# Performance work log

Measured on AMD Instinct MI355X. Metric: run time of the kernel, lower is better.

## Reference

```python
import jax, jax.numpy as jnp
from jax import lax
import numpy as np

DN = ('NCDHW', 'OIDHW', 'NCDHW')
EPS = 1e-3  # BatchNorm1d eps=0.001
GRID = (41, 512, 512)  # spatial_shape [40,512,512] + [1,0,0]


def _block(x, mask, w, gamma, beta, rmean, rvar, stride, padding):
    # Regular (non-submanifold) sparse conv computes the same values as a dense
    # conv on the zero-filled grid; active OUTPUT sites are exactly those reached
    # by any active input site through the kernel window. BN+ReLU act only on
    # active sites (inactive sites stay exactly 0), hence the mask multiply.
    y = lax.conv_general_dilated(x, w, stride, padding, dimension_numbers=DN)
    k1 = jnp.ones((1, 1) + w.shape[2:], x.dtype)
    m = lax.conv_general_dilated(mask, k1, stride, padding, dimension_numbers=DN)
    m = (m > 0).astype(x.dtype)
    inv = gamma / jnp.sqrt(rvar + EPS)
    scale = inv.reshape(1, -1, 1, 1, 1)
    shift = (beta - rmean * inv).reshape(1, -1, 1, 1, 1)
    return jax.nn.relu(y * scale + shift) * m, m


def setup_inputs() -> dict:
    key = jax.random.key(0)
    NV, B = 120000, 2
    kf, kb, kz, ky, kx, kp = jax.random.split(key, 6)
    voxel_features = jax.random.normal(kf, (NV, 3), jnp.float32)
    coors = jnp.stack([
        jax.random.randint(kb, (NV,), 0, B, jnp.int32),
        jax.random.randint(kz, (NV,), 0, 40, jnp.int32),
        jax.random.randint(ky, (NV,), 0, 512, jnp.int32),
        jax.random.randint(kx, (NV,), 0, 512, jnp.int32)], axis=1)
    inp = {"voxel_features": voxel_features, "coors": coors, "batch_size": B}
    chans = [(3, 16, (3, 3, 3)), (16, 32, (3, 3, 3)), (32, 64, (3, 3, 3)), (64, 64, (3, 1, 1))]
    for i, (ci, co, k) in enumerate(chans, 1):
        kw, kg, kbb, km, kv = jax.random.split(jax.random.fold_in(kp, i), 5)
        fan = ci * k[0] * k[1] * k[2]
        inp[f"w{i}"] = jax.random.normal(kw, (co, ci) + k, jnp.float32) / np.sqrt(fan).astype(np.float32)
        inp[f"g{i}"] = jax.random.uniform(kg, (co,), jnp.float32, 0.5, 1.5)
        inp[f"bb{i}"] = jax.random.normal(kbb, (co,), jnp.float32) * 0.1
        inp[f"rm{i}"] = jax.random.normal(km, (co,), jnp.float32) * 0.1
        inp[f"rv{i}"] = jax.random.uniform(kv, (co,), jnp.float32, 0.5, 1.5)
    return inp


def reference(voxel_features, coors, batch_size,
              w1, g1, bb1, rm1, rv1,
              w2, g2, bb2, rm2, rv2,
              w3, g3, bb3, rm3, rv3,
              w4, g4, bb4, rm4, rv4):
    D, H, W = GRID
    C = voxel_features.shape[1]
    b, z, y, x = coors[:, 0], coors[:, 1], coors[:, 2], coors[:, 3]
    dense = jnp.zeros((batch_size, C, D, H, W), voxel_features.dtype)
    dense = dense.at[b, :, z, y, x].add(voxel_features)  # scatter voxels to grid
    mask = jnp.zeros((batch_size, 1, D, H, W), voxel_features.dtype).at[b, 0, z, y, x].set(1.0)
    h, m = _block(dense, mask, w1, g1, bb1, rm1, rv1, (2, 2, 2), [(1, 1), (1, 1), (1, 1)])
    h, m = _block(h, m, w2, g2, bb2, rm2, rv2, (2, 2, 2), [(1, 1), (1, 1), (1, 1)])
    h, m = _block(h, m, w3, g3, bb3, rm3, rv3, (2, 2, 2), [(0, 0), (1, 1), (1, 1)])
    h, m = _block(h, m, w4, g4, bb4, rm4, rv4, (2, 1, 1), [(0, 0), (0, 0), (0, 0)])
    N, Co, Dd, Hh, Ww = h.shape  # [B, 64, 2, 64, 64]
    return h.reshape(N, Co * Dd, Hh, Ww)
```

## Files before the change

kernel.cpp:

```cpp
#include <hip/hip_runtime.h>

#define EPS 1e-3f


static __device__ __forceinline__ unsigned f2bf(float f) {
    unsigned u = __float_as_uint(f);
    return (u + 0x7FFFu + ((u >> 16) & 1u)) >> 16;
}

typedef _Float16 f16x8 __attribute__((ext_vector_type(8)));
typedef float f32x4 __attribute__((ext_vector_type(4)));
typedef float f32x16 __attribute__((ext_vector_type(16)));

__global__ __launch_bounds__(256) void repack_prezero(
    const float* __restrict__ g1, const float* __restrict__ b1,
    const float* __restrict__ rm1, const float* __restrict__ rv1,
    const float* __restrict__ w2, const float* __restrict__ g2, const float* __restrict__ b2,
    const float* __restrict__ rm2, const float* __restrict__ rv2,
    const float* __restrict__ w3, const float* __restrict__ g3, const float* __restrict__ b3,
    const float* __restrict__ rm3, const float* __restrict__ rv3,
    const float* __restrict__ w4, const float* __restrict__ g4, const float* __restrict__ b4,
    const float* __restrict__ rm4, const float* __restrict__ rv4,
    _Float16* __restrict__ wB2, _Float16* __restrict__ wB3,
    _Float16* __restrict__ wB4, float* __restrict__ shb,
    const int* __restrict__ coors, int NV, unsigned short* __restrict__ y1)
{
    if (blockIdx.x >= 321) {
        const int i = (blockIdx.x - 321) * 256 + threadIdx.x;
        if (i < NV) {
            const int b = coors[4 * i + 0];
            const int z = coors[4 * i + 1];
            const int y = coors[4 * i + 2];
            const int x = coors[4 * i + 3];
            int ozv[2], nz = 0, oyv[2], ny = 0, oxv[2], nx = 0;
#pragma unroll
            for (int k = 0; k < 3; ++k) {
                int t = z + 1 - k;
                if (t >= 0 && !(t & 1)) { int o = t >> 1; if (o < 21) ozv[nz++] = o; }
            }
#pragma unroll
            for (int k = 0; k < 3; ++k) {
                int t = y + 1 - k;
                if (t >= 0 && !(t & 1)) { int o = t >> 1; if (o < 256) oyv[ny++] = o; }
            }
#pragma unroll
            for (int k = 0; k < 3; ++k) {
                int t = x + 1 - k;
                if (t >= 0 && !(t & 1)) { int o = t >> 1; if (o < 256) oxv[nx++] = o; }
            }
            const uint4 zz = {0u, 0u, 0u, 0u};
            for (int a = 0; a < nz; ++a)
                for (int bb = 0; bb < ny; ++bb)
                    for (int c = 0; c < nx; ++c) {
                        const int sp = ozv[a] * 65536 + oyv[bb] * 256 + oxv[c];
                        uint4* p = (uint4*)(y1 + (size_t)(b * 1376256 + sp) * 16);
                        p[0] = zz;
                        p[1] = zz;
                    }
        }
        asm volatile("s_waitcnt vmcnt(0)" ::: "memory");
        return;
    }

    const int i = blockIdx.x * 256 + threadIdx.x;
    if (i < 13824) {
        const int j = i & 7, lane = (i >> 3) & 63, tap = i >> 9;
        const int oc = lane & 31;
        const int cin = (lane >> 5) * 8 + j;
        const float inv = g2[oc] * rsqrtf(rv2[oc] + EPS);
        wB2[i] = (_Float16)(w2[(oc * 16 + cin) * 27 + tap] * inv);
    } else if (i >= 14336 && i < 69632) {
        const int j2 = i - 14336;
        const int j = j2 & 7, lane = (j2 >> 3) & 63, t = (j2 >> 9) & 3, tap = j2 >> 11;
        const int q = lane >> 4, n = lane & 15;
        const int oc = t * 16 + n;
        const int cin = q * 8 + j;
        const float inv = g3[oc] * rsqrtf(rv3[oc] + EPS);
        wB3[j2] = (_Float16)(w3[(oc * 32 + cin) * 27 + tap] * inv);
    } else if (i >= 69632 && i < 81920) {
        const int j2 = i - 69632;
        const int j = j2 & 7, lane = (j2 >> 3) & 63, t = (j2 >> 9) & 3, c = j2 >> 11;
        const int q = lane >> 4, n = lane & 15;
        const int oc = t * 16 + n;
        const int k = c * 32 + q * 8 + j;
        const int dz = k >> 6, cin = k & 63;
        const float inv = g4[oc] * rsqrtf(rv4[oc] + EPS);
        wB4[j2] = (_Float16)(w4[(oc * 64 + cin) * 3 + dz] * inv);
    } else if (i >= 81920 && i < 82112) {
        const int j = i - 81920;
        if (j < 32) {
            const float inv = g2[j] * rsqrtf(rv2[j] + EPS);
            shb[j] = b2[j] - rm2[j] * inv;
        } else if (j < 96) {
            const int o = j - 32;
            const float inv = g3[o] * rsqrtf(rv3[o] + EPS);
            shb[j] = b3[o] - rm3[o] * inv;
        } else if (j < 160) {
            const int o = j - 96;
            const float inv = g4[o] * rsqrtf(rv4[o] + EPS);
            shb[j] = b4[o] - rm4[o] * inv;
        } else if (j < 176) {
            const int o = j - 160;
            shb[j] = g1[o] * rsqrtf(rv1[o] + EPS);
        } else if (j < 192) {
            const int o = j - 176;
            const float inv = g1[o] * rsqrtf(rv1[o] + EPS);
            shb[j] = b1[o] - rm1[o] * inv;
        }
    }
}

__global__ __launch_bounds__(256) void scatter_l1(
    const float* __restrict__ vf, const int* __restrict__ coors, int NV,
    const float* __restrict__ w1, const float* __restrict__ shb,
    unsigned short* __restrict__ y1, unsigned char* __restrict__ m1)
{
    __shared__ float ws[16 * 3 * 27];
    for (int e = threadIdx.x; e < 16 * 3 * 27; e += 256)
        ws[e] = w1[e] * shb[160 + e / 81];
    __syncthreads();

    const int gid = blockIdx.x * 256 + threadIdx.x;
    const int i = gid >> 3;
    const int oc2 = gid & 7;
    if (i < NV) {
        const int oc = oc2 * 2;

        const int b = coors[4 * i + 0];
        const int z = coors[4 * i + 1];
        const int y = coors[4 * i + 2];
        const int x = coors[4 * i + 3];
        const float f0 = vf[3 * i + 0];
        const float f1 = vf[3 * i + 1];
        const float f2 = vf[3 * i + 2];

        int ozv[2], kzv[2], nz = 0;
        int oyv[2], kyv[2], ny = 0;
        int oxv[2], kxv[2], nx = 0;
#pragma unroll
        for (int k = 0; k < 3; ++k) {
            int t = z + 1 - k;
            if (t >= 0 && !(t & 1)) { int o = t >> 1; if (o < 21) { ozv[nz] = o; kzv[nz] = k; ++nz; } }
        }
#pragma unroll
        for (int k = 0; k < 3; ++k) {
            int t = y + 1 - k;
            if (t >= 0 && !(t & 1)) { int o = t >> 1; if (o < 256) { oyv[ny] = o; kyv[ny] = k; ++ny; } }
        }
#pragma unroll
        for (int k = 0; k < 3; ++k) {
            int t = x + 1 - k;
            if (t >= 0 && !(t & 1)) { int o = t >> 1; if (o < 256) { oxv[nx] = o; kxv[nx] = k; ++nx; } }
        }

        for (int a = 0; a < nz; ++a)
            for (int bb = 0; bb < ny; ++bb)
                for (int c = 0; c < nx; ++c) {
                    const int oz = ozv[a], oy = oyv[bb], ox = oxv[c];
                    const int tap = (kzv[a] * 3 + kyv[bb]) * 3 + kxv[c];
                    const int sp = oz * 65536 + oy * 256 + ox;
                    if (oc2 == 0) m1[b * 1376256 + sp] = 1;
                    const float s0 = ws[oc * 81 + tap] * f0 + ws[oc * 81 + 27 + tap] * f1 +
                                     ws[oc * 81 + 54 + tap] * f2;
                    const float s1 = ws[(oc + 1) * 81 + tap] * f0 +
                                     ws[(oc + 1) * 81 + 27 + tap] * f1 +
                                     ws[(oc + 1) * 81 + 54 + tap] * f2;
                    const unsigned pk = f2bf(s0) | (f2bf(s1) << 16);
                    unsigned* addr = (unsigned*)(y1 + (size_t)(b * 1376256 + sp) * 16 +
                                                 oc2 * 2);
                    asm volatile("global_atomic_pk_add_bf16 %0, %1, off"
                                 : : "v"(addr), "v"(pk) : "memory");
                }
    }
    asm volatile("s_waitcnt vmcnt(0)" ::: "memory");
}

__global__ __launch_bounds__(256) void h1_pass(
    uint4* __restrict__ y1b, const unsigned char* __restrict__ m1,
    const float* __restrict__ shb, float* __restrict__ m2)
{
    const int idx = blockIdx.x * 256 + threadIdx.x;
    if (m1[idx]) {
        uint4 u0 = y1b[idx * 2], u1 = y1b[idx * 2 + 1];
        const unsigned d[8] = {u0.x, u0.y, u0.z, u0.w, u1.x, u1.y, u1.z, u1.w};
        unsigned o[8];
#pragma unroll
        for (int j = 0; j < 8; ++j) {
            const int c0 = 2 * j;
            const float vlo = __uint_as_float(d[j] << 16);
            const float vhi = __uint_as_float(d[j] & 0xFFFF0000u);
            const float v0 = fmaxf(vlo + shb[176 + c0], 0.f);
            const float v1 = fmaxf(vhi + shb[176 + c0 + 1], 0.f);
            o[j] = __builtin_bit_cast(unsigned, __builtin_amdgcn_cvt_pkrtz(v0, v1));
        }
        uint4 w0, w1;
        w0.x = o[0]; w0.y = o[1]; w0.z = o[2]; w0.w = o[3];
        w1.x = o[4]; w1.y = o[5]; w1.z = o[6]; w1.w = o[7];
        y1b[idx * 2] = w0;
        y1b[idx * 2 + 1] = w1;
    } else {
        const uint4 zz = {0u, 0u, 0u, 0u};
        y1b[idx * 2] = zz;
        y1b[idx * 2 + 1] = zz;
    }

    if (idx < 360448) {
        const int b = idx / 180224;
        const int r = idx - b * 180224;
        const int oz = r >> 14, r2 = r & 16383, oy = r2 >> 7, ox = r2 & 127;
        const int iz0 = 2 * oz - 1, iyb = 2 * oy - 1, ixb = 2 * ox - 1;
        unsigned msum = 0;
#pragma unroll
        for (int kz = 0; kz < 3; ++kz) {
            const int iz = iz0 + kz;
#pragma unroll
            for (int ky = 0; ky < 3; ++ky) {
                const int iy = iyb + ky;
#pragma unroll
                for (int kx = 0; kx < 3; ++kx) {
                    const int ix = ixb + kx;
                    if ((unsigned)iz < 21u && (unsigned)iy < 256u &&
                        (unsigned)ix < 256u)
                        msum |= m1[b * 1376256 + iz * 65536 + iy * 256 + ix];
                }
            }
        }
        m2[idx] = msum ? 1.f : 0.f;
    }
}

__global__ __launch_bounds__(256) void build_m3(
    const float* __restrict__ m2, float* __restrict__ m3)
{
    const int idx = blockIdx.x * 256 + threadIdx.x;
    if (idx >= 40960) return;
    const int b = idx / 20480;
    const int r = idx - b * 20480;
    const int oz = r >> 12, r2 = r & 4095, oy = r2 >> 6, ox = r2 & 63;
    const int iz0 = 2 * oz, iyb = 2 * oy - 1, ixb = 2 * ox - 1;

    float msum = 0.f;
#pragma unroll
    for (int kz = 0; kz < 3; ++kz) {
        const int iz = iz0 + kz;
#pragma unroll
        for (int ky = 0; ky < 3; ++ky) {
            const int iy = iyb + ky;
#pragma unroll
            for (int kx = 0; kx < 3; ++kx) {
                const int ix = ixb + kx;
                if ((unsigned)iy < 128u && (unsigned)ix < 128u)
                    msum += m2[b * 180224 + iz * 16384 + iy * 128 + ix];
            }
        }
    }
    m3[idx] = msum > 0.f ? 1.f : 0.f;
}

__global__ __launch_bounds__(256) __attribute__((amdgpu_waves_per_eu(4, 8)))
void conv_l2(
    const unsigned char* __restrict__ h1,
    const uint4* __restrict__ wB2,
    const float* __restrict__ m2, const float* __restrict__ shb,
    _Float16* __restrict__ h2h)
{
    const int tid = threadIdx.x;
    const int gw = blockIdx.x * 4 + (tid >> 6);
    const int lane = tid & 63;
    const int m = lane & 31, h = lane >> 5;

    const int plane = gw >> 9;
    const int rem = gw & 511;
    const int oy = rem >> 2;
    const int ox0 = (rem & 3) * 32;
    const int b = plane / 11, oz = plane % 11;
    const int iz0 = 2 * oz - 1, iyb = 2 * oy - 1;
    const int ixm = 2 * (ox0 + m) - 1;
    const int bbase = b * 1376256;
    const int qoff = h * 16;

    f32x16 acc;
#pragma unroll
    for (int r = 0; r < 16; ++r) acc[r] = 0.f;

    uint4 buf[13];
    bool  val[13];
#pragma unroll
    for (int t = 0; t < 13; ++t) {
        const int kz = t / 9, ky = (t / 3) % 3, kx = t % 3;
        const int iz = iz0 + kz, iy = iyb + ky, ix = ixm + kx;
        const bool v = (unsigned)iz < 21u && (unsigned)iy < 256u &&
                       (unsigned)ix < 256u;
        const int cell = bbase + iz * 65536 + iy * 256 + ix;
        buf[t] = *(const uint4*)(h1 + (v ? (cell * 32 + qoff) : 0));
        val[t] = v;
    }

#pragma unroll
    for (int tap = 0; tap < 27; ++tap) {
        const int s = tap % 13;
        uint4 ua = buf[s];
        if (!val[s]) { ua.x = 0; ua.y = 0; ua.z = 0; ua.w = 0; }
        if (tap + 13 < 27) {
            const int t2 = tap + 13;
            const int kz = t2 / 9, ky = (t2 / 3) % 3, kx = t2 % 3;
            const int iz = iz0 + kz, iy = iyb + ky, ix = ixm + kx;
            const bool v = (unsigned)iz < 21u && (unsigned)iy < 256u &&
                           (unsigned)ix < 256u;
            const int cell = bbase + iz * 65536 + iy * 256 + ix;
            buf[s] = *(const uint4*)(h1 + (v ? (cell * 32 + qoff) : 0));
            val[s] = v;
        }
        const f16x8 af = __builtin_bit_cast(f16x8, ua);
        const f16x8 bf = __builtin_bit_cast(f16x8, wB2[tap * 64 + lane]);
        acc = __builtin_amdgcn_mfma_f32_32x32x16_f16(af, bf, acc, 0, 0, 0);
    }

    const int oc = lane & 31;
#pragma unroll
    for (int r = 0; r < 16; ++r) {
        const int row = (r & 3) + 8 * (r >> 2) + 4 * h;
        const int px = ox0 + row;
        const int spo = oz * 16384 + oy * 128 + px;
        const float mv = m2[b * 180224 + spo];
        const size_t cbase = (size_t)(b * 180224 + spo) * 32;
        h2h[cbase + oc] = (_Float16)(fmaxf(acc[r] + shb[oc], 0.f) * mv);
    }
}

__global__ __launch_bounds__(256) __attribute__((amdgpu_waves_per_eu(4, 8)))
void conv_l3(
    const unsigned char* __restrict__ h2h,
    const uint4* __restrict__ wB3,
    const float* __restrict__ m3, const float* __restrict__ shb,
    _Float16* __restrict__ h3h)
{
    const int tid = threadIdx.x;
    const int gw = blockIdx.x * 4 + (tid >> 6);
    const int lane = tid & 63;
    const int m = lane & 15, q = lane >> 4;

    const int plane = gw >> 8;
    const int rem = gw & 255;
    const int oy = rem >> 2;
    const int ox0 = (rem & 3) * 16;
    const int b = plane / 5, oz = plane % 5;
    const int iz0 = 2 * oz, iyb = 2 * oy - 1;
    const int ixm = 2 * (ox0 + m) - 1;
    const int bbase = b * 180224;
    const int qoff = q * 16;

    f32x4 acc[4];
#pragma unroll
    for (int t = 0; t < 4; ++t) acc[t] = (f32x4){0.f, 0.f, 0.f, 0.f};

    uint4 buf[9];
    bool  val[9];
#pragma unroll
    for (int t = 0; t < 9; ++t) {
        const int ky = (t / 3) % 3, kx = t % 3;
        const int iz = iz0 + t / 9, iy = iyb + ky, ix = ixm + kx;
        const bool v = (unsigned)iy < 128u && (unsigned)ix < 128u;
        const int cell = bbase + iz * 16384 + iy * 128 + ix;
        buf[t] = *(const uint4*)(h2h + (v ? (cell * 64 + qoff) : 0));
        val[t] = v;
    }

#pragma unroll
    for (int tap = 0; tap < 27; ++tap) {
        const int s = tap % 9;
        uint4 ua = buf[s];
        if (!val[s]) { ua.x = 0; ua.y = 0; ua.z = 0; ua.w = 0; }
        if (tap + 9 < 27) {
            const int t2 = tap + 9;
            const int kz = t2 / 9, ky = (t2 / 3) % 3, kx = t2 % 3;
            const int iz = iz0 + kz, iy = iyb + ky, ix = ixm + kx;
            const bool v = (unsigned)iy < 128u && (unsigned)ix < 128u;
            const int cell = bbase + iz * 16384 + iy * 128 + ix;
            buf[s] = *(const uint4*)(h2h + (v ? (cell * 64 + qoff) : 0));
            val[s] = v;
        }
        const f16x8 af = __builtin_bit_cast(f16x8, ua);
#pragma unroll
        for (int t = 0; t < 4; ++t) {
            const f16x8 bf = __builtin_bit_cast(f16x8, wB3[(tap * 4 + t) * 64 + lane]);
            acc[t] = __builtin_amdgcn_mfma_f32_16x16x32_f16(af, bf, acc[t], 0, 0, 0);
        }
    }

    const int n = lane & 15;
#pragma unroll
    for (int r = 0; r < 4; ++r) {
        const int px = ox0 + q * 4 + r;
        const int spo = oz * 4096 + oy * 64 + px;
        const float mv = m3[b * 20480 + spo];
        const size_t cb = (size_t)(b * 20480 + spo) * 64;
#pragma unroll
        for (int t = 0; t < 4; ++t) {
            const int oc = t * 16 + n;
            h3h[cb + oc] = (_Float16)(fmaxf(acc[t][r] + shb[32 + oc], 0.f) * mv);
        }
    }
}

__global__ __launch_bounds__(256) __attribute__((amdgpu_waves_per_eu(4, 8)))
void conv_l4(
    const unsigned char* __restrict__ h3h,
    const uint4* __restrict__ wB4,
    const float* __restrict__ m3, const float* __restrict__ shb,
    float* __restrict__ out)
{
    const int tid = threadIdx.x;
    const int gw = blockIdx.x * 4 + (tid >> 6);
    const int lane = tid & 63;
    const int m = lane & 15, q = lane >> 4;

    const int b = gw >> 9, od = (gw >> 8) & 1;
    const int oy = (gw >> 2) & 63, ox0 = (gw & 3) * 16;
    const int cellbase = (b * 5 + 2 * od) * 4096 + oy * 64 + ox0 + m;

    f32x4 acc[4];
#pragma unroll
    for (int t = 0; t < 4; ++t) acc[t] = (f32x4){0.f, 0.f, 0.f, 0.f};

#pragma unroll
    for (int c = 0; c < 6; ++c) {
        const int dz = c >> 1;
        const size_t addr = (size_t)(cellbase + dz * 4096) * 128 +
                            (c & 1) * 64 + q * 16;
        const uint4 ua = *(const uint4*)(h3h + addr);
        const f16x8 af = __builtin_bit_cast(f16x8, ua);
#pragma unroll
        for (int t = 0; t < 4; ++t) {
            const f16x8 bf = __builtin_bit_cast(f16x8, wB4[(c * 4 + t) * 64 + lane]);
            acc[t] = __builtin_amdgcn_mfma_f32_16x16x32_f16(af, bf, acc[t], 0, 0, 0);
        }
    }

    const int n = lane & 15;
#pragma unroll
    for (int r = 0; r < 4; ++r) {
        const int px = ox0 + q * 4 + r;
        const int spo = oy * 64 + px;
        const float msum = m3[(b * 5 + 2 * od + 0) * 4096 + spo] +
                           m3[(b * 5 + 2 * od + 1) * 4096 + spo] +
                           m3[(b * 5 + 2 * od + 2) * 4096 + spo];
        const float mv = msum > 0.f ? 1.f : 0.f;
#pragma unroll
        for (int t = 0; t < 4; ++t) {
            const int oc = t * 16 + n;
            out[((b * 64 + oc) * 2 + od) * 4096 + spo] =
                fmaxf(acc[t][r] + shb[96 + oc], 0.f) * mv;
        }
    }
}

extern "C" void kernel_launch(void* const* d_in, const int* in_sizes, int n_in,
                              void* d_out, int out_size, void* d_ws, size_t ws_size,
                              hipStream_t stream)
{
    const float* vf    = (const float*)d_in[0];
    const int*   coors = (const int*)d_in[1];
    const float* w1 = (const float*)d_in[3];
    const float* g1 = (const float*)d_in[4];
    const float* b1 = (const float*)d_in[5];
    const float* rm1 = (const float*)d_in[6];
    const float* rv1 = (const float*)d_in[7];
    const float* w2 = (const float*)d_in[8];
    const float* g2 = (const float*)d_in[9];
    const float* b2 = (const float*)d_in[10];
    const float* rm2 = (const float*)d_in[11];
    const float* rv2 = (const float*)d_in[12];
    const float* w3 = (const float*)d_in[13];
    const float* g3 = (const float*)d_in[14];
    const float* b3 = (const float*)d_in[15];
    const float* rm3 = (const float*)d_in[16];
    const float* rv3 = (const float*)d_in[17];
    const float* w4 = (const float*)d_in[18];
    const float* g4 = (const float*)d_in[19];
    const float* b4 = (const float*)d_in[20];
    const float* rm4 = (const float*)d_in[21];
    const float* rv4 = (const float*)d_in[22];

    const int NV = in_sizes[0] / 3;

    float* ws = (float*)d_ws;
    float* y1  = ws;
    float* m1f = y1 + 22020096;
    float* h2h = m1f + 2752512;
    float* m2  = h2h + 5767168;
    float* h3h = m2 + 360448;
    float* m3  = h3h + 1310720;
    float* wB2 = m3 + 40960;
    float* wB3 = wB2 + 7168;
    float* wB4 = wB3 + 27648;
    float* shb = wB4 + 6144;

    unsigned char* m1 = (unsigned char*)m1f;

    (void)hipMemsetAsync(m1, 0, 2752512, stream);

    const int pzBlocks = (NV + 255) / 256;
    repack_prezero<<<321 + pzBlocks, 256, 0, stream>>>(
        g1, b1, rm1, rv1,
        w2, g2, b2, rm2, rv2, w3, g3, b3, rm3, rv3,
        w4, g4, b4, rm4, rv4,
        (_Float16*)wB2, (_Float16*)wB3, (_Float16*)wB4, shb,
        coors, NV, (unsigned short*)y1);
    scatter_l1<<<(NV * 8 + 255) / 256, 256, 0, stream>>>(vf, coors, NV, w1, shb,
                                                         (unsigned short*)y1, m1);
    h1_pass<<<10752, 256, 0, stream>>>((uint4*)y1, m1, shb, m2);
    build_m3<<<160, 256, 0, stream>>>(m2, m3);
    conv_l2<<<2816, 256, 0, stream>>>((const unsigned char*)y1, (const uint4*)wB2,
                                      m2, shb, (_Float16*)h2h);
    conv_l3<<<640, 256, 0, stream>>>((const unsigned char*)h2h, (const uint4*)wB3,
                                     m3, shb, (_Float16*)h3h);
    conv_l4<<<256, 256, 0, stream>>>((const unsigned char*)h3h, (const uint4*)wB4,
                                     m3, shb, (float*)d_out);
}
```

Before: 225.8 us.

## Fuse layer-1 BN/ReLU/mask into conv_l2 and drop the dense h1 pass

Removes the full-grid h1_pass that rewrote every layer-1 output cell. conv_l2 now reads the raw bf16 accumulator, adds the shift, applies ReLU, converts to fp16 and zeroes inactive sites using the m1 byte mask, all on the fly. That saves a large read-modify-write sweep over y1, at the cost of extra per-tap VALU work and mask loads inside conv_l2. The m1 memset and the m3 zeroing move into the repack kernel. m3 is now built by scattering from active m2 sites inside a combined masks pass, which removes the separate build_m3 launch.

After: 206.1 us. 8.7% less time.

```diff
diff --git a/kernel.cpp b/kernel.cpp
--- a/kernel.cpp
+++ b/kernel.cpp
@@ -23,10 +23,11 @@
     const float* __restrict__ rm4, const float* __restrict__ rv4,
     _Float16* __restrict__ wB2, _Float16* __restrict__ wB3,
     _Float16* __restrict__ wB4, float* __restrict__ shb,
-    const int* __restrict__ coors, int NV, unsigned short* __restrict__ y1)
-{
-    if (blockIdx.x >= 321) {
-        const int i = (blockIdx.x - 321) * 256 + threadIdx.x;
+    const int* __restrict__ coors, int NV, unsigned short* __restrict__ y1,
+    unsigned char* __restrict__ m1, float* __restrict__ m3)
+{
+    if (blockIdx.x >= 1034) {
+        const int i = (blockIdx.x - 1034) * 256 + threadIdx.x;
         if (i < NV) {
             const int b = coors[4 * i + 0];
             const int z = coors[4 * i + 1];
@@ -59,6 +60,16 @@
                     }
         }
         asm volatile("s_waitcnt vmcnt(0)" ::: "memory");
+        return;
+    }
+    if (blockIdx.x >= 321) {
+        const int idx16 = (blockIdx.x - 321) * 256 + threadIdx.x;
+        const uint4 zz = {0u, 0u, 0u, 0u};
+        if (idx16 < 172033) {
+            ((uint4*)m1)[idx16] = zz;
+        } else if (idx16 < 182273) {
+            ((uint4*)m3)[idx16 - 172033] = zz;
+        }
         return;
     }
 
@@ -175,71 +186,16 @@
     asm volatile("s_waitcnt vmcnt(0)" ::: "memory");
 }
 
-__global__ __launch_bounds__(256) void h1_pass(
-    uint4* __restrict__ y1b, const unsigned char* __restrict__ m1,
-    const float* __restrict__ shb, float* __restrict__ m2)
+__global__ __launch_bounds__(256) void masks_pass(
+    const unsigned char* __restrict__ m1, float* __restrict__ m2,
+    float* __restrict__ m3)
 {
     const int idx = blockIdx.x * 256 + threadIdx.x;
-    if (m1[idx]) {
-        uint4 u0 = y1b[idx * 2], u1 = y1b[idx * 2 + 1];
-        const unsigned d[8] = {u0.x, u0.y, u0.z, u0.w, u1.x, u1.y, u1.z, u1.w};
-        unsigned o[8];
-#pragma unroll
-        for (int j = 0; j < 8; ++j) {
-            const int c0 = 2 * j;
-            const float vlo = __uint_as_float(d[j] << 16);
-            const float vhi = __uint_as_float(d[j] & 0xFFFF0000u);
-            const float v0 = fmaxf(vlo + shb[176 + c0], 0.f);
-            const float v1 = fmaxf(vhi + shb[176 + c0 + 1], 0.f);
-            o[j] = __builtin_bit_cast(unsigned, __builtin_amdgcn_cvt_pkrtz(v0, v1));
-        }
-        uint4 w0, w1;
-        w0.x = o[0]; w0.y = o[1]; w0.z = o[2]; w0.w = o[3];
-        w1.x = o[4]; w1.y = o[5]; w1.z = o[6]; w1.w = o[7];
-        y1b[idx * 2] = w0;
-        y1b[idx * 2 + 1] = w1;
-    } else {
-        const uint4 zz = {0u, 0u, 0u, 0u};
-        y1b[idx * 2] = zz;
-        y1b[idx * 2 + 1] = zz;
-    }
-
-    if (idx < 360448) {
-        const int b = idx / 180224;
-        const int r = idx - b * 180224;
-        const int oz = r >> 14, r2 = r & 16383, oy = r2 >> 7, ox = r2 & 127;
-        const int iz0 = 2 * oz - 1, iyb = 2 * oy - 1, ixb = 2 * ox - 1;
-        unsigned msum = 0;
-#pragma unroll
-        for (int kz = 0; kz < 3; ++kz) {
-            const int iz = iz0 + kz;
-#pragma unroll
-            for (int ky = 0; ky < 3; ++ky) {
-                const int iy = iyb + ky;
-#pragma unroll
-                for (int kx = 0; kx < 3; ++kx) {
-                    const int ix = ixb + kx;
-                    if ((unsigned)iz < 21u && (unsigned)iy < 256u &&
-                        (unsigned)ix < 256u)
-                        msum |= m1[b * 1376256 + iz * 65536 + iy * 256 + ix];
-                }
-            }
-        }
-        m2[idx] = msum ? 1.f : 0.f;
-    }
-}
-
-__global__ __launch_bounds__(256) void build_m3(
-    const float* __restrict__ m2, float* __restrict__ m3)
-{
-    const int idx = blockIdx.x * 256 + threadIdx.x;
-    if (idx >= 40960) return;
-    const int b = idx / 20480;
-    const int r = idx - b * 20480;
-    const int oz = r >> 12, r2 = r & 4095, oy = r2 >> 6, ox = r2 & 63;
-    const int iz0 = 2 * oz, iyb = 2 * oy - 1, ixb = 2 * ox - 1;
-
-    float msum = 0.f;
+    const int b = idx / 180224;
+    const int r = idx - b * 180224;
+    const int oz = r >> 14, r2 = r & 16383, oy = r2 >> 7, ox = r2 & 127;
+    const int iz0 = 2 * oz - 1, iyb = 2 * oy - 1, ixb = 2 * ox - 1;
+    unsigned msum = 0;
 #pragma unroll
     for (int kz = 0; kz < 3; ++kz) {
         const int iz = iz0 + kz;
@@ -249,17 +205,42 @@
 #pragma unroll
             for (int kx = 0; kx < 3; ++kx) {
                 const int ix = ixb + kx;
-                if ((unsigned)iy < 128u && (unsigned)ix < 128u)
-                    msum += m2[b * 180224 + iz * 16384 + iy * 128 + ix];
+                if ((unsigned)iz < 21u && (unsigned)iy < 256u &&
+                    (unsigned)ix < 256u)
+                    msum |= m1[b * 1376256 + iz * 65536 + iy * 256 + ix];
             }
         }
     }
-    m3[idx] = msum > 0.f ? 1.f : 0.f;
+    m2[idx] = msum ? 1.f : 0.f;
+
+    if (msum) {
+        int ozv[2], nz = 0, oyv[2], ny = 0, oxv[2], nx = 0;
+#pragma unroll
+        for (int k = 0; k < 3; ++k) {
+            int t = oz - k;
+            if (t >= 0 && !(t & 1)) { int o = t >> 1; if (o < 5) ozv[nz++] = o; }
+        }
+#pragma unroll
+        for (int k = 0; k < 3; ++k) {
+            int t = oy + 1 - k;
+            if (t >= 0 && !(t & 1)) { int o = t >> 1; if (o < 64) oyv[ny++] = o; }
+        }
+#pragma unroll
+        for (int k = 0; k < 3; ++k) {
+            int t = ox + 1 - k;
+            if (t >= 0 && !(t & 1)) { int o = t >> 1; if (o < 64) oxv[nx++] = o; }
+        }
+        for (int a = 0; a < nz; ++a)
+            for (int bb = 0; bb < ny; ++bb)
+                for (int c = 0; c < nx; ++c)
+                    m3[b * 20480 + ozv[a] * 4096 + oyv[bb] * 64 + oxv[c]] = 1.0f;
+    }
 }
 
 __global__ __launch_bounds__(256) __attribute__((amdgpu_waves_per_eu(4, 8)))
 void conv_l2(
-    const unsigned char* __restrict__ h1,
+    const unsigned char* __restrict__ y1c,
+    const unsigned char* __restrict__ m1,
     const uint4* __restrict__ wB2,
     const float* __restrict__ m2, const float* __restrict__ shb,
     _Float16* __restrict__ h2h)
@@ -279,12 +260,20 @@
     const int bbase = b * 1376256;
     const int qoff = h * 16;
 
+    float s1v[8];
+    {
+        const float4* sp = (const float4*)(shb + 176 + h * 8);
+        const float4 a0 = sp[0], a1 = sp[1];
+        s1v[0] = a0.x; s1v[1] = a0.y; s1v[2] = a0.z; s1v[3] = a0.w;
+        s1v[4] = a1.x; s1v[5] = a1.y; s1v[6] = a1.z; s1v[7] = a1.w;
+    }
+
     f32x16 acc;
 #pragma unroll
     for (int r = 0; r < 16; ++r) acc[r] = 0.f;
 
     uint4 buf[13];
-    bool  val[13];
+    unsigned char mb[13];
 #pragma unroll
     for (int t = 0; t < 13; ++t) {
         const int kz = t / 9, ky = (t / 3) % 3, kx = t % 3;
@@ -292,15 +281,15 @@
         const bool v = (unsigned)iz < 21u && (unsigned)iy < 256u &&
                        (unsigned)ix < 256u;
         const int cell = bbase + iz * 65536 + iy * 256 + ix;
-        buf[t] = *(const uint4*)(h1 + (v ? (cell * 32 + qoff) : 0));
-        val[t] = v;
+        buf[t] = *(const uint4*)(y1c + (v ? (cell * 32 + qoff) : 0));
+        mb[t] = m1[v ? cell : 2752512];
     }
 
 #pragma unroll
     for (int tap = 0; tap < 27; ++tap) {
         const int s = tap % 13;
-        uint4 ua = buf[s];
-        if (!val[s]) { ua.x = 0; ua.y = 0; ua.z = 0; ua.w = 0; }
+        const uint4 ua = buf[s];
+        const unsigned char mbv = mb[s];
         if (tap + 13 < 27) {
             const int t2 = tap + 13;
             const int kz = t2 / 9, ky = (t2 / 3) % 3, kx = t2 % 3;
@@ -308,10 +297,23 @@
             const bool v = (unsigned)iz < 21u && (unsigned)iy < 256u &&
                            (unsigned)ix < 256u;
             const int cell = bbase + iz * 65536 + iy * 256 + ix;
-            buf[s] = *(const uint4*)(h1 + (v ? (cell * 32 + qoff) : 0));
-            val[s] = v;
-        }
-        const f16x8 af = __builtin_bit_cast(f16x8, ua);
+            buf[s] = *(const uint4*)(y1c + (v ? (cell * 32 + qoff) : 0));
+            mb[s] = m1[v ? cell : 2752512];
+        }
+        const bool act = mbv != 0;
+        unsigned od[4];
+        const unsigned dvs[4] = {ua.x, ua.y, ua.z, ua.w};
+#pragma unroll
+        for (int jj = 0; jj < 4; ++jj) {
+            const unsigned dv = dvs[jj];
+            const float vlo = fmaxf(__uint_as_float(dv << 16) + s1v[2 * jj], 0.f);
+            const float vhi = fmaxf(__uint_as_float(dv & 0xFFFF0000u) + s1v[2 * jj + 1], 0.f);
+            const unsigned pk =
+                __builtin_bit_cast(unsigned, __builtin_amdgcn_cvt_pkrtz(vlo, vhi));
+            od[jj] = act ? pk : 0u;
+        }
+        const uint4 uc = {od[0], od[1], od[2], od[3]};
+        const f16x8 af = __builtin_bit_cast(f16x8, uc);
         const f16x8 bf = __builtin_bit_cast(f16x8, wB2[tap * 64 + lane]);
         acc = __builtin_amdgcn_mfma_f32_32x32x16_f16(af, bf, acc, 0, 0, 0);
     }
@@ -498,21 +500,18 @@
 
     unsigned char* m1 = (unsigned char*)m1f;
 
-    (void)hipMemsetAsync(m1, 0, 2752512, stream);
-
     const int pzBlocks = (NV + 255) / 256;
-    repack_prezero<<<321 + pzBlocks, 256, 0, stream>>>(
+    repack_prezero<<<1034 + pzBlocks, 256, 0, stream>>>(
         g1, b1, rm1, rv1,
         w2, g2, b2, rm2, rv2, w3, g3, b3, rm3, rv3,
         w4, g4, b4, rm4, rv4,
         (_Float16*)wB2, (_Float16*)wB3, (_Float16*)wB4, shb,
-        coors, NV, (unsigned short*)y1);
+        coors, NV, (unsigned short*)y1, m1, m3);
     scatter_l1<<<(NV * 8 + 255) / 256, 256, 0, stream>>>(vf, coors, NV, w1, shb,
                                                          (unsigned short*)y1, m1);
-    h1_pass<<<10752, 256, 0, stream>>>((uint4*)y1, m1, shb, m2);
-    build_m3<<<160, 256, 0, stream>>>(m2, m3);
-    conv_l2<<<2816, 256, 0, stream>>>((const unsigned char*)y1, (const uint4*)wB2,
-                                      m2, shb, (_Float16*)h2h);
+    masks_pass<<<1408, 256, 0, stream>>>(m1, m2, m3);
+    conv_l2<<<2816, 256, 0, stream>>>((const unsigned char*)y1, m1,
+                                      (const uint4*)wB2, m2, shb, (_Float16*)h2h);
     conv_l3<<<640, 256, 0, stream>>>((const unsigned char*)h2h, (const uint4*)wB3,
                                      m3, shb, (_Float16*)h3h);
     conv_l4<<<256, 256, 0, stream>>>((const unsigned char*)h3h, (const uint4*)wB4,
```
